# Kernel optimization log

Hardware: AMD Instinct MI355X
Metric: run time of the kernel (lower is better)

The kernel has to match this reference:

```python
import jax, jax.numpy as jnp
import numpy as np


def setup_inputs() -> dict:
    key = jax.random.key(0)
    k1, k2, k3, k4 = jax.random.split(key, 4)
    B, S, E, A = 4, 4096, 1024, 1024
    embedded = jax.random.normal(k1, (B, S, E), dtype=jnp.float32)
    # nn.Linear(E, A, bias=False) weights, stored as [E, A] so y = x @ W
    Wk = jax.random.normal(k2, (E, A), dtype=jnp.float32) * (E ** -0.5)
    Wq = jax.random.normal(k3, (E, A), dtype=jnp.float32) * (E ** -0.5)
    Wv = jax.random.normal(k4, (E, A), dtype=jnp.float32) * (E ** -0.5)
    return {"embedded": embedded, "Wk": Wk, "Wq": Wq, "Wv": Wv}


def reference(embedded, Wk, Wq, Wv):
    # K, Q, V projections: [B, S, A]
    K = embedded @ Wk
    Q = embedded @ Wq
    V = embedded @ Wv
    A = K.shape[-1]
    S = embedded.shape[1]
    # causal scores [B, S, S]
    scores = jnp.einsum("bqa,bka->bqk", Q, K) / jnp.sqrt(jnp.float32(A))
    causal = jnp.tril(jnp.ones((S, S), dtype=bool))
    scores = jnp.where(causal, scores, -jnp.inf)
    probs = jax.nn.softmax(scores, axis=-1)
    out = jnp.einsum("bqk,bka->bqa", probs, V)
    # torch.round(out, decimals=4)
    return jnp.round(out, 4)
```

## Files before the change

kernel.cpp:

```cpp
#include <hip/hip_runtime.h>
#include <hip/hip_fp16.h>

typedef __attribute__((ext_vector_type(4))) float f32x4;
typedef __attribute__((ext_vector_type(8))) short s16x8;
typedef __attribute__((ext_vector_type(4))) short s16x4;
typedef unsigned short u16;
typedef unsigned int u32;

__device__ __forceinline__ u16 f2bf(float f) {
    union { float f; unsigned u; } x; x.f = f;
    return (u16)((x.u + 0x7fffu + ((x.u >> 16) & 1u)) >> 16);
}

__device__ __forceinline__ void ld16(const void* g, void* l) {
    __builtin_amdgcn_global_load_lds(
        (const __attribute__((address_space(1))) unsigned int*)g,
        (__attribute__((address_space(3))) unsigned int*)l, 16, 0, 0);
}

__device__ __forceinline__ void kstep64(const u16* gA, const u16* gB, const u16* gC,
                                        long lda, long ldb,
                                        u16* sA, u16* sB,
                                        int wm, int wn, int lm, int lg,
                                        f32x4 acc0[4][4], f32x4 acc1[4][4])
{
    const int t = threadIdx.x;
    __syncthreads();
#pragma unroll
    for (int p = 0; p < 4; p++) {
        ld16(gA + (long)p * 32 * lda, sA + p * 2048 + t * 8);
        ld16(gB + (long)p * 32 * ldb, sB + p * 2048 + t * 8);
        ld16(gC + (long)p * 32 * ldb, sB + 8192 + p * 2048 + t * 8);
    }
    __syncthreads();

#pragma unroll
    for (int s = 0; s < 2; s++) {
        s16x8 af[4], bf[4], cf[4];
        const int co = (((s * 4 + lg) ^ (lm & 7)) << 3);
#pragma unroll
        for (int i = 0; i < 4; i++) {
            af[i] = *(const s16x8*)&sA[(wm + i * 16 + lm) * 64 + co];
            bf[i] = *(const s16x8*)&sB[(wn + i * 16 + lm) * 64 + co];
            cf[i] = *(const s16x8*)&sB[8192 + (wn + i * 16 + lm) * 64 + co];
        }
#pragma unroll
        for (int i = 0; i < 4; i++)
#pragma unroll
            for (int j = 0; j < 4; j++) {
                acc0[i][j] = __builtin_amdgcn_mfma_f32_16x16x32_bf16(af[i], bf[j], acc0[i][j], 0, 0, 0);
                acc1[i][j] = __builtin_amdgcn_mfma_f32_16x16x32_bf16(af[i], cf[j], acc1[i][j], 0, 0, 0);
            }
    }
}

__device__ __forceinline__ void gemm_core64(const u16* A, long lda,
                                            const u16* B0, const u16* B1, long ldb,
                                            int m0, int kEnd,
                                            f32x4 acc0[4][4], f32x4 acc1[4][4],
                                            u16* sA, u16* sB)
{
    const int t    = threadIdx.x;
    const int lane = t & 63;
    const int wave = t >> 6;
    const int wm   = (wave & 1) << 6;
    const int wn   = (wave >> 1) << 6;
    const int lm   = lane & 15;
    const int lg   = lane >> 4;
    const int sr   = t >> 3;
    const int sc   = (((t & 7) ^ ((t >> 3) & 7)) << 3);
    const u16* gA0 = A + (long)(m0 + sr) * lda + sc;
    const u16* gB0 = B0 + (long)sr * ldb + sc;
    const u16* gC0 = B1 + (long)sr * ldb + sc;

    for (int k0 = 0; k0 < kEnd; k0 += 64)
        kstep64(gA0 + k0, gB0 + k0, gC0 + k0, lda, ldb,
                sA, sB, wm, wn, lm, lg, acc0, acc1);
}

__global__ void convert_x(const float* __restrict__ X, u16* __restrict__ Xb) {
    long idx = ((long)blockIdx.x * 256 + threadIdx.x) * 4;
    f32x4 v = *(const f32x4*)&X[idx];
    s16x4 o;
    o.x = (short)f2bf(v.x); o.y = (short)f2bf(v.y);
    o.z = (short)f2bf(v.z); o.w = (short)f2bf(v.w);
    *(s16x4*)&Xb[idx] = o;
}

__global__ void convert_w(const float* __restrict__ Wk, const float* __restrict__ Wq,
                          const float* __restrict__ Wv,
                          u16* __restrict__ Wkt, u16* __restrict__ Wqt, u16* __restrict__ Wvt) {
    const float* W; u16* O;
    if (blockIdx.y == 0)      { W = Wk; O = Wkt; }
    else if (blockIdx.y == 1) { W = Wq; O = Wqt; }
    else                      { W = Wv; O = Wvt; }
    __shared__ u16 tile[64][65];
    int k0 = (blockIdx.x >> 4) << 6, n0 = (blockIdx.x & 15) << 6;
    int t = threadIdx.x;
    int rr = t >> 4, cc = (t & 15) << 2;
#pragma unroll
    for (int i = 0; i < 4; i++) {
        int row = rr + i * 16;
        f32x4 v = *(const f32x4*)&W[(long)(k0 + row) * 1024 + n0 + cc];
        tile[row][cc + 0] = f2bf(v.x); tile[row][cc + 1] = f2bf(v.y);
        tile[row][cc + 2] = f2bf(v.z); tile[row][cc + 3] = f2bf(v.w);
    }
    __syncthreads();
#pragma unroll
    for (int i = 0; i < 4; i++) {
        int row = rr + i * 16;
        s16x4 pk;
        pk.x = (short)tile[cc + 0][row]; pk.y = (short)tile[cc + 1][row];
        pk.z = (short)tile[cc + 2][row]; pk.w = (short)tile[cc + 3][row];
        *(s16x4*)&O[(long)(n0 + row) * 1024 + k0 + cc] = pk;
    }
}

__device__ __forceinline__ void stage_half64(const u16* gbase, u16* lbase,
                                             int kt, int h, int t) {
    const u16* g = gbase + (long)(h * 128) * 1024 + kt * 64;
    u16* l = lbase + h * 8192 + t * 8;
    ld16(g, l);
    ld16(g + 64 * 1024, l + 4096);
}

__device__ __forceinline__ void read_A8(const u16* sA, int arow, int ih,
                                        int co0, int co1, s16x8 af[4][2]) {
#pragma unroll
    for (int i = 0; i < 4; i++) {
        af[i][0] = *(const s16x8*)&sA[(arow + (ih * 4 + i) * 16) * 64 + co0];
        af[i][1] = *(const s16x8*)&sA[(arow + (ih * 4 + i) * 16) * 64 + co1];
    }
}

__device__ __forceinline__ void read_B8(const u16* sB, int brow,
                                        int co0, int co1, s16x8 bf[4][2]) {
#pragma unroll
    for (int j = 0; j < 4; j++) {
        bf[j][0] = *(const s16x8*)&sB[(brow + j * 16) * 64 + co0];
        bf[j][1] = *(const s16x8*)&sB[(brow + j * 16) * 64 + co1];
    }
}

__device__ __forceinline__ void mfma16q(f32x4 acc[8][4], const s16x8 af[4][2],
                                        const s16x8 bf[4][2], int ih, int jh) {
    __builtin_amdgcn_s_setprio(1);
#pragma unroll
    for (int i = 0; i < 4; i++)
#pragma unroll
        for (int j = 0; j < 2; j++)
#pragma unroll
            for (int s = 0; s < 2; s++)
                acc[ih * 4 + i][jh * 2 + j] = __builtin_amdgcn_mfma_f32_16x16x32_bf16(
                    af[i][s], bf[jh * 2 + j][s], acc[ih * 4 + i][jh * 2 + j], 0, 0, 0);
    __builtin_amdgcn_s_setprio(0);
}

#define PH_BAR()  __builtin_amdgcn_s_barrier()
#define PH_LGKM() asm volatile("s_waitcnt lgkmcnt(0)" ::: "memory")

__global__ __launch_bounds__(512, 2) void proj_all8(const u16* __restrict__ X,
                                                    const u16* __restrict__ Wqt,
                                                    const u16* __restrict__ Wkt,
                                                    const u16* __restrict__ Wvt,
                                                    u16* __restrict__ Qb,
                                                    u16* __restrict__ Kb,
                                                    u16* __restrict__ Vt) {
    __shared__ u16 lds[65536];
    const int bx  = blockIdx.x;
    const int z   = bx >> 8;
    const int rem = bx & 255;
    const int m0  = (rem >> 2) << 8;
    const int n0  = (rem & 3) << 8;
    const u16* Wt = (z == 0) ? Wqt : (z == 1) ? Wkt : Wvt;

    const int t  = threadIdx.x;
    const int sr = t >> 3;
    const int sc = ((t & 7) ^ (sr & 7)) << 3;
    const u16* Ast = X  + (long)(m0 + sr) * 1024 + sc;
    const u16* Bst = Wt + (long)(n0 + sr) * 1024 + sc;
    u16* sA0 = lds;
    u16* sA1 = lds + 16384;
    u16* sB0 = lds + 32768;
    u16* sB1 = lds + 49152;

    const int lane = t & 63, w = t >> 6;
    const int wr = w >> 2, wc = w & 3;
    const int lm = lane & 15, lg = lane >> 4;
    const int arow = wr * 128 + lm;
    const int brow = wc * 64 + lm;
    const int co0 = ((lg) ^ (lm & 7)) << 3;
    const int co1 = ((4 + lg) ^ (lm & 7)) << 3;

    f32x4 acc[8][4] = {};
    s16x8 af[4][2], bf[4][2];

    stage_half64(Bst, sB0, 0, 0, t); stage_half64(Bst, sB0, 0, 1, t);
    stage_half64(Ast, sA0, 0, 0, t); stage_half64(Ast, sA0, 0, 1, t);
    stage_half64(Bst, sB1, 1, 0, t); stage_half64(Bst, sB1, 1, 1, t);
    stage_half64(Ast, sA1, 1, 0, t);
    asm volatile("s_waitcnt vmcnt(6)" ::: "memory");
    PH_BAR();

#pragma unroll 1
    for (int it = 0; it < 8; it++) {
        const int  tO   = 2 * it + 1;
        const bool more = (it < 7);
        read_A8(sA0, arow, 0, co0, co1, af);
        read_B8(sB0, brow, co0, co1, bf);
        stage_half64(Ast, sA1, tO, 1, t);
        PH_BAR(); PH_LGKM();
        mfma16q(acc, af, bf, 0, 0);
        PH_BAR();
        if (more) stage_half64(Bst, sB0, tO + 1, 0, t);
        PH_BAR(); PH_LGKM();
        mfma16q(acc, af, bf, 0, 1);
        PH_BAR();
        read_A8(sA0, arow, 1, co0, co1, af);
        if (more) stage_half64(Bst, sB0, tO + 1, 1, t);
        PH_BAR(); PH_LGKM();
        mfma16q(acc, af, bf, 1, 0);
        PH_BAR();
        if (more) stage_half64(Ast, sA0, tO + 1, 0, t);
        PH_BAR(); PH_LGKM();
        mfma16q(acc, af, bf, 1, 1);
        if (more) asm volatile("s_waitcnt vmcnt(6)" ::: "memory");
        else      asm volatile("s_waitcnt vmcnt(0)" ::: "memory");
        PH_BAR();
        read_A8(sA1, arow, 0, co0, co1, af);
        read_B8(sB1, brow, co0, co1, bf);
        if (more) stage_half64(Ast, sA0, tO + 1, 1, t);
        PH_BAR(); PH_LGKM();
        mfma16q(acc, af, bf, 0, 0);
        PH_BAR();
        if (more) stage_half64(Bst, sB1, tO + 2, 0, t);
        PH_BAR(); PH_LGKM();
        mfma16q(acc, af, bf, 0, 1);
        PH_BAR();
        read_A8(sA1, arow, 1, co0, co1, af);
        if (more) stage_half64(Bst, sB1, tO + 2, 1, t);
        PH_BAR(); PH_LGKM();
        mfma16q(acc, af, bf, 1, 0);
        PH_BAR();
        if (more) stage_half64(Ast, sA1, tO + 2, 0, t);
        PH_BAR(); PH_LGKM();
        mfma16q(acc, af, bf, 1, 1);
        if (more) asm volatile("s_waitcnt vmcnt(6)" ::: "memory");
        PH_BAR();
    }

    if (z < 2) {
        u16* O = (z == 0) ? Qb : Kb;
#pragma unroll
        for (int i = 0; i < 8; i++)
#pragma unroll
            for (int j = 0; j < 4; j++)
#pragma unroll
                for (int r = 0; r < 4; r++) {
                    int row = m0 + wr * 128 + i * 16 + lg * 4 + r;
                    int col = n0 + wc * 64 + j * 16 + lm;
                    O[(long)row * 1024 + col] = f2bf(acc[i][j][r]);
                }
    } else {
#pragma unroll
        for (int i = 0; i < 8; i++)
#pragma unroll
            for (int j = 0; j < 4; j++) {
                int row0 = m0 + wr * 128 + i * 16 + lg * 4;
                int col  = n0 + wc * 64 + j * 16 + lm;
                int b = row0 >> 12, s = row0 & 4095;
                s16x4 p0;
                p0.x = (short)f2bf(acc[i][j][0]); p0.y = (short)f2bf(acc[i][j][1]);
                p0.z = (short)f2bf(acc[i][j][2]); p0.w = (short)f2bf(acc[i][j][3]);
                *(s16x4*)&Vt[(long)b * 4194304 + (long)col * 4096 + s] = p0;
            }
    }
}

__global__ __launch_bounds__(256, 2) void sgemm_causal(const u16* __restrict__ Q,
                                                       const u16* __restrict__ K,
                                                       u16* __restrict__ S,
                                                       float* __restrict__ l) {
    __shared__ u16 sA[8192], sB[16384];
    int b  = blockIdx.x / 272;
    int tt = blockIdx.x % 272;
    int it = (int)(2.0f * sqrtf((float)tt + 1.0f)) - 1;
    if (it > 31) it = 31;
    if (it < 0) it = 0;
    while (it < 31 && (((it + 2) * (it + 2)) >> 2) <= tt) ++it;
    while (it > 0 && (((it + 1) * (it + 1)) >> 2) > tt) --it;
    int jp  = tt - (((it + 1) * (it + 1)) >> 2);
    int jt0 = jp * 2, jt1 = jt0 + 1;
    bool valid1 = (jt1 <= it);

    const u16* A  = Q + (long)b * 4194304;
    const u16* Kp = K + (long)b * 4194304;
    f32x4 acc0[4][4] = {}, acc1[4][4] = {};
    gemm_core64(A, 1024, Kp + (long)jt0 * 131072, Kp + (long)jt1 * 131072, 1024,
                it * 128, 1024, acc0, acc1, sA, sB);

    long tribase = (long)(b * 528 + ((it * (it + 1)) >> 1));
    u16* Sp0 = S + (tribase + jt0) * 16384;
    u16* Sp1 = S + (tribase + jt1) * 16384;
    int lane = threadIdx.x & 63, wave = threadIdx.x >> 6;
    int wm = (wave & 1) << 6, wn = (wave >> 1) << 6, lm = lane & 15, lg = lane >> 4;
    const float LOG2E = 1.44269504088896f;

    float rs[4][4];
#pragma unroll
    for (int i = 0; i < 4; i++)
#pragma unroll
        for (int r = 0; r < 4; r++) rs[i][r] = 0.0f;

#pragma unroll
    for (int i = 0; i < 4; i++)
#pragma unroll
        for (int j = 0; j < 4; j++)
#pragma unroll
            for (int r = 0; r < 4; r++) {
                int ri = wm + i * 16 + lg * 4 + r;
                int cj = wn + j * 16 + lm;
                int gi = it * 128 + ri;
                float p0 = (jt0 * 128 + cj > gi) ? 0.0f
                         : exp2f((acc0[i][j][r] * 0.03125f - 16.0f) * LOG2E);
                Sp0[ri * 128 + cj] = f2bf(p0);
                rs[i][r] += p0;
                if (valid1) {
                    float p1 = (jt1 * 128 + cj > gi) ? 0.0f
                             : exp2f((acc1[i][j][r] * 0.03125f - 16.0f) * LOG2E);
                    Sp1[ri * 128 + cj] = f2bf(p1);
                    rs[i][r] += p1;
                }
            }

#pragma unroll
    for (int i = 0; i < 4; i++)
#pragma unroll
        for (int r = 0; r < 4; r++) {
            float s = rs[i][r];
            s += __shfl_xor(s, 1, 64);
            s += __shfl_xor(s, 2, 64);
            s += __shfl_xor(s, 4, 64);
            s += __shfl_xor(s, 8, 64);
            if (lm == 0)
                atomicAdd(&l[b * 4096 + it * 128 + wm + i * 16 + lg * 4 + r], s);
        }
}

__global__ __launch_bounds__(256, 2) void pv_gemm(const u16* __restrict__ P,
                                                  const u16* __restrict__ Vt,
                                                  const float* __restrict__ l,
                                                  float* __restrict__ Out) {
    __shared__ u16 sA[8192], sB[16384];
    int g  = blockIdx.x;
    int it = (g < 256) ? (31 - (g >> 4)) : ((g - 256) >> 4);
    int rem = g & 15;
    int b   = rem >> 2;
    int atp = rem & 3;

    const int t    = threadIdx.x;
    const int lane = t & 63;
    const int wave = t >> 6;
    const int wm   = (wave & 1) << 6;
    const int wn   = (wave >> 1) << 6;
    const int lm   = lane & 15;
    const int lg   = lane >> 4;
    const int sr   = t >> 3;
    const int sc   = (((t & 7) ^ ((t >> 3) & 7)) << 3);

    const u16* Pbase = P + (long)(b * 528 + ((it * (it + 1)) >> 1)) * 16384;
    const u16* gA0 = Pbase + sr * 128 + sc;
    const u16* gB0 = Vt + (long)b * 4194304 + (long)(atp * 256 + sr) * 4096 + sc;
    const u16* gC0 = gB0 + (long)128 * 4096;

    f32x4 acc0[4][4] = {}, acc1[4][4] = {};
    for (int jt = 0; jt <= it; jt++) {
        long aoff = (long)jt * 16384;
        long boff = (long)jt * 128;
#pragma unroll
        for (int kk = 0; kk < 128; kk += 64)
            kstep64(gA0 + aoff + kk, gB0 + boff + kk, gC0 + boff + kk,
                    128, 4096, sA, sB, wm, wn, lm, lg, acc0, acc1);
    }

#pragma unroll
    for (int i = 0; i < 4; i++)
#pragma unroll
        for (int r = 0; r < 4; r++) {
            int gi = it * 128 + wm + i * 16 + lg * 4 + r;
            float scale = 1.0f / l[b * 4096 + gi];
#pragma unroll
            for (int j = 0; j < 4; j++) {
                int ga = atp * 256 + wn + j * 16 + lm;
                float* o = &Out[((long)b * 4096 + gi) * 1024 + ga];
                o[0]   = acc0[i][j][r] * scale;
                o[128] = acc1[i][j][r] * scale;
            }
        }
}

extern "C" void kernel_launch(void* const* d_in, const int* in_sizes, int n_in,
                              void* d_out, int out_size, void* d_ws, size_t ws_size,
                              hipStream_t stream) {
    const float* X  = (const float*)d_in[0];
    const float* Wk = (const float*)d_in[1];
    const float* Wq = (const float*)d_in[2];
    const float* Wv = (const float*)d_in[3];
    float* Out = (float*)d_out;

    char* w = (char*)d_ws;
    u16*   Qb   = (u16*)(w);
    u16*   Kb   = (u16*)(w + 33554432);
    u16*   Vt   = (u16*)(w + 67108864);
    float* l    = (float*)(w + 100663296);
    u16*   Xb   = (u16*)(w + 100728832);
    u16*   Wqt  = (u16*)(w + 134283264);
    u16*   Wkt  = (u16*)(w + 136380416);
    u16*   Wvt  = (u16*)(w + 138477568);
    u16*   S    = (u16*)(w + 100728832);

    hipMemsetAsync(l, 0, 65536, stream);
    convert_x<<<16384, 256, 0, stream>>>(X, Xb);
    convert_w<<<dim3(256, 3), 256, 0, stream>>>(Wk, Wq, Wv, Wkt, Wqt, Wvt);
    proj_all8<<<768, 512, 0, stream>>>(Xb, Wqt, Wkt, Wvt, Qb, Kb, Vt);
    sgemm_causal<<<1088, 256, 0, stream>>>(Qb, Kb, S, l);
    pv_gemm<<<512, 256, 0, stream>>>(S, Vt, l, Out);
}
```

Measured before the change: 426.8 us.

## Rework projection GEMM pipeline: split B reads, drop lgkm waits, remap blocks

New measurement: 415.7 us. -2.6%, faster.

```diff
diff --git a/kernel.cpp b/kernel.cpp
--- a/kernel.cpp
+++ b/kernel.cpp
@@ -133,10 +133,10 @@
     }
 }
 
-__device__ __forceinline__ void read_B8(const u16* sB, int brow,
+__device__ __forceinline__ void read_B4(const u16* sB, int brow, int jp,
                                         int co0, int co1, s16x8 bf[4][2]) {
 #pragma unroll
-    for (int j = 0; j < 4; j++) {
+    for (int j = 2 * jp; j < 2 * jp + 2; j++) {
         bf[j][0] = *(const s16x8*)&sB[(brow + j * 16) * 64 + co0];
         bf[j][1] = *(const s16x8*)&sB[(brow + j * 16) * 64 + co1];
     }
@@ -156,8 +156,7 @@
     __builtin_amdgcn_s_setprio(0);
 }
 
-#define PH_BAR()  __builtin_amdgcn_s_barrier()
-#define PH_LGKM() asm volatile("s_waitcnt lgkmcnt(0)" ::: "memory")
+#define ABAR() asm volatile("s_barrier" ::: "memory")
 
 __global__ __launch_bounds__(512, 2) void proj_all8(const u16* __restrict__ X,
                                                     const u16* __restrict__ Wqt,
@@ -167,7 +166,7 @@
                                                     u16* __restrict__ Kb,
                                                     u16* __restrict__ Vt) {
     __shared__ u16 lds[65536];
-    const int bx  = blockIdx.x;
+    const int bx  = ((blockIdx.x & 7) * 96) + (blockIdx.x >> 3);
     const int z   = bx >> 8;
     const int rem = bx & 255;
     const int m0  = (rem >> 2) << 8;
@@ -198,55 +197,56 @@
     stage_half64(Bst, sB0, 0, 0, t); stage_half64(Bst, sB0, 0, 1, t);
     stage_half64(Ast, sA0, 0, 0, t); stage_half64(Ast, sA0, 0, 1, t);
     stage_half64(Bst, sB1, 1, 0, t); stage_half64(Bst, sB1, 1, 1, t);
-    stage_half64(Ast, sA1, 1, 0, t);
-    asm volatile("s_waitcnt vmcnt(6)" ::: "memory");
-    PH_BAR();
+    asm volatile("s_waitcnt vmcnt(4)" ::: "memory");
+    ABAR();
 
 #pragma unroll 1
     for (int it = 0; it < 8; it++) {
         const int  tO   = 2 * it + 1;
         const bool more = (it < 7);
         read_A8(sA0, arow, 0, co0, co1, af);
-        read_B8(sB0, brow, co0, co1, bf);
+        read_B4(sB0, brow, 0, co0, co1, bf);
+        stage_half64(Ast, sA1, tO, 0, t);
+        ABAR();
+        mfma16q(acc, af, bf, 0, 0);
+        ABAR();
+        read_B4(sB0, brow, 1, co0, co1, bf);
         stage_half64(Ast, sA1, tO, 1, t);
-        PH_BAR(); PH_LGKM();
+        ABAR();
+        mfma16q(acc, af, bf, 0, 1);
+        ABAR();
+        read_A8(sA0, arow, 1, co0, co1, af);
+        if (more) stage_half64(Bst, sB0, tO + 1, 0, t);
+        ABAR();
+        mfma16q(acc, af, bf, 1, 0);
+        ABAR();
+        if (more) stage_half64(Bst, sB0, tO + 1, 1, t);
+        ABAR();
+        mfma16q(acc, af, bf, 1, 1);
+        if (more) asm volatile("s_waitcnt vmcnt(4)" ::: "memory");
+        else      asm volatile("s_waitcnt vmcnt(0)" ::: "memory");
+        ABAR();
+        read_A8(sA1, arow, 0, co0, co1, af);
+        read_B4(sB1, brow, 0, co0, co1, bf);
+        if (more) stage_half64(Ast, sA0, tO + 1, 0, t);
+        ABAR();
         mfma16q(acc, af, bf, 0, 0);
-        PH_BAR();
-        if (more) stage_half64(Bst, sB0, tO + 1, 0, t);
-        PH_BAR(); PH_LGKM();
+        ABAR();
+        read_B4(sB1, brow, 1, co0, co1, bf);
+        if (more) stage_half64(Ast, sA0, tO + 1, 1, t);
+        ABAR();
         mfma16q(acc, af, bf, 0, 1);
-        PH_BAR();
-        read_A8(sA0, arow, 1, co0, co1, af);
-        if (more) stage_half64(Bst, sB0, tO + 1, 1, t);
-        PH_BAR(); PH_LGKM();
+        ABAR();
+        read_A8(sA1, arow, 1, co0, co1, af);
+        if (more) stage_half64(Bst, sB1, tO + 2, 0, t);
+        ABAR();
         mfma16q(acc, af, bf, 1, 0);
-        PH_BAR();
-        if (more) stage_half64(Ast, sA0, tO + 1, 0, t);
-        PH_BAR(); PH_LGKM();
+        ABAR();
+        if (more) stage_half64(Bst, sB1, tO + 2, 1, t);
+        ABAR();
         mfma16q(acc, af, bf, 1, 1);
-        if (more) asm volatile("s_waitcnt vmcnt(6)" ::: "memory");
-        else      asm volatile("s_waitcnt vmcnt(0)" ::: "memory");
-        PH_BAR();
-        read_A8(sA1, arow, 0, co0, co1, af);
-        read_B8(sB1, brow, co0, co1, bf);
-        if (more) stage_half64(Ast, sA0, tO + 1, 1, t);
-        PH_BAR(); PH_LGKM();
-        mfma16q(acc, af, bf, 0, 0);
-        PH_BAR();
-        if (more) stage_half64(Bst, sB1, tO + 2, 0, t);
-        PH_BAR(); PH_LGKM();
-        mfma16q(acc, af, bf, 0, 1);
-        PH_BAR();
-        read_A8(sA1, arow, 1, co0, co1, af);
-        if (more) stage_half64(Bst, sB1, tO + 2, 1, t);
-        PH_BAR(); PH_LGKM();
-        mfma16q(acc, af, bf, 1, 0);
-        PH_BAR();
-        if (more) stage_half64(Ast, sA1, tO + 2, 0, t);
-        PH_BAR(); PH_LGKM();
-        mfma16q(acc, af, bf, 1, 1);
-        if (more) asm volatile("s_waitcnt vmcnt(6)" ::: "memory");
-        PH_BAR();
+        if (more) asm volatile("s_waitcnt vmcnt(4)" ::: "memory");
+        ABAR();
     }
 
     if (z < 2) {
```
